# Kernel tuning notes

Hardware: AMD Instinct MI355X
Metric: run time of the kernel (lower is better)

Reference implementation:

```python
import jax, jax.numpy as jnp
import numpy as np

C = 512
NUM_HEADS = 8
RF = 4          # reduction_factor
GROUPS = 8      # min(8, C//8)
EPS = 1e-5


def _pos_enc(h, w, c):
    # matches torch _create_positional_encoding; c must be divisible by 4
    y = jnp.arange(h, dtype=jnp.float32)[:, None] * jnp.ones((1, w), jnp.float32)
    x = jnp.ones((h, 1), jnp.float32) * jnp.arange(w, dtype=jnp.float32)[None, :]
    div = jnp.exp(jnp.arange(0, c // 2, 2, dtype=jnp.float32) * (-np.log(10000.0) / (c // 2)))  # [c//4]
    d = div[:, None, None]
    sy, cy = jnp.sin(y[None] * d), jnp.cos(y[None] * d)   # [c//4,h,w]
    sx, cx = jnp.sin(x[None] * d), jnp.cos(x[None] * d)
    pe = jnp.stack([sy, cy, sx, cx], axis=1).reshape(c, h, w)  # interleaved 0::4..3::4
    return pe[None] * 0.01


def _group_norm(x, w, b):
    B, Cc, H, W = x.shape
    g = x.reshape(B, GROUPS, -1)
    m = g.mean(-1, keepdims=True)
    v = g.var(-1, keepdims=True)
    g = (g - m) / jnp.sqrt(v + EPS)
    return g.reshape(B, Cc, H, W) * w[None, :, None, None] + b[None, :, None, None]


def setup_inputs() -> dict:
    key = jax.random.key(0)
    ks = jax.random.split(key, 4)
    B, H, W = 1, 256, 256
    x = jax.random.normal(ks[0], (B, C, H, W), jnp.float32)
    qkv_w = jax.random.normal(ks[1], (3 * C, C), jnp.float32) * 0.02
    proj_w = jax.random.normal(ks[2], (C, C), jnp.float32) * 0.02
    gamma = jax.random.normal(ks[3], (1,), jnp.float32)
    return {
        "x": x,
        "gn_weight": jnp.ones((C,), jnp.float32),
        "gn_bias": jnp.zeros((C,), jnp.float32),
        "qkv_w": qkv_w,
        "proj_w": proj_w,
        "proj_b": jnp.zeros((C,), jnp.float32),
        "gamma": gamma,
        "temperature": jnp.ones((NUM_HEADS, 1, 1), jnp.float32),
    }


def reference(x, gn_weight, gn_bias, qkv_w, proj_w, proj_b, gamma, temperature):
    B, Cc, H, W = x.shape
    hd = Cc // NUM_HEADS
    identity = x
    xn = _group_norm(x, gn_weight, gn_bias)
    # spatial reduction (AvgPool2d k=4 s=4); H,W > 32 in this config
    Hr, Wr = H // RF, W // RF
    xr = xn.reshape(B, Cc, Hr, RF, Wr, RF).mean(axis=(3, 5))
    xr = xr + _pos_enc(Hr, Wr, Cc)
    qkv = jnp.einsum('oc,bchw->bohw', qkv_w, xr)  # 1x1 conv, no bias
    q, k, v = jnp.split(qkv, 3, axis=1)
    N = Hr * Wr
    q = q.reshape(B, NUM_HEADS, hd, N) * (hd ** -0.5) * temperature[None]
    k = k.reshape(B, NUM_HEADS, hd, N)
    v = v.reshape(B, NUM_HEADS, hd, N)
    # chunked attention in torch == plain softmax attention (chunking over queries)
    attn = jax.nn.softmax(jnp.einsum('bhdn,bhdm->bhnm', q, k), axis=-1)
    out = jnp.einsum('bhnm,bhdm->bhdn', attn, v).reshape(B, Cc, Hr, Wr)
    out = jax.image.resize(out, (B, Cc, H, W), method='bilinear')  # align_corners=False
    out = jnp.einsum('oc,bchw->bohw', proj_w, out) + proj_b[None, :, None, None]
    # dropout in eval mode is identity
    return identity + gamma * out
```

## Files before the change

### kernel.cpp

```cpp
#include <hip/hip_runtime.h>
#include <hip/hip_bf16.h>


typedef __attribute__((ext_vector_type(4))) short short4v;
typedef __attribute__((ext_vector_type(8))) short short8v;
typedef __attribute__((ext_vector_type(4))) float f32x4;
typedef __attribute__((ext_vector_type(4))) unsigned int u32x4;

#define MFMA16(a, b, c) __builtin_amdgcn_mfma_f32_16x16x32_bf16(a, b, c, 0, 0, 0)

__device__ __forceinline__ unsigned short bf16r(float f) {
    unsigned int u = __builtin_bit_cast(unsigned int, f);
    u += 0x7fffu + ((u >> 16) & 1u);
    return (unsigned short)(u >> 16);
}
__device__ __forceinline__ float bff(unsigned short s) {
    unsigned int u = ((unsigned int)s) << 16;
    return __builtin_bit_cast(float, u);
}
__device__ __forceinline__ unsigned int fbits(float f) {
    return __builtin_bit_cast(unsigned int, f);
}

typedef const __attribute__((address_space(1))) unsigned int guint;
typedef __attribute__((address_space(3))) unsigned int luint;
__device__ __forceinline__ void gload16(const void* g, void* l) {
    __builtin_amdgcn_global_load_lds((guint*)g, (luint*)l, 16, 0, 0);
}

__global__ __launch_bounds__(256) void k_wconv(const float* __restrict__ qkv_w,
                                               const float* __restrict__ proj_w,
                                               const float* __restrict__ temp,
                                               unsigned short* __restrict__ wq_b,
                                               unsigned short* __restrict__ wp_b) {
    int idx = blockIdx.x * 256 + threadIdx.x;
    const int NQ = 1536 * 512;
    if (idx < NQ) {
        int o = idx >> 9;
        float sc = (o < 512) ? temp[o >> 6] * 0.125f : 1.0f;
        wq_b[idx] = bf16r(qkv_w[idx] * sc);
    } else {
        int j = idx - NQ;
        wp_b[j] = bf16r(proj_w[j]);
    }
}

__global__ __launch_bounds__(256) void k_pool(const float* __restrict__ x,
                                              float* __restrict__ xp,
                                              float* __restrict__ partials) {
    int hr = blockIdx.x;
    int c  = blockIdx.y;
    int t = threadIdx.x;
    int r = t >> 6, wq = t & 63;
    const float4* src = (const float4*)(x + (size_t)c * 65536 + (size_t)(4 * hr + r) * 256 + 4 * wq);
    float4 v = *src;
    float s4 = v.x + v.y + v.z + v.w;
    float q4 = v.x * v.x + v.y * v.y + v.z * v.z + v.w * v.w;

    __shared__ float sm[256];
    __shared__ float wq4[4];
    sm[t] = s4;
    float qq = q4;
#pragma unroll
    for (int off = 1; off < 64; off <<= 1) qq += __shfl_xor(qq, off, 64);
    if ((t & 63) == 0) wq4[t >> 6] = qq;
    __syncthreads();
    if (t < 64) {
        float cs = sm[t] + sm[64 + t] + sm[128 + t] + sm[192 + t];
        xp[(size_t)c * 4096 + hr * 64 + t] = cs * (1.0f / 16.0f);
        float ts = cs;
#pragma unroll
        for (int off = 1; off < 64; off <<= 1) ts += __shfl_xor(ts, off, 64);
        if (t == 0) {
            int g = c >> 6;
            int slot = (c & 63) * 64 + hr;
            partials[(size_t)(g * 4096 + slot) * 2 + 0] = ts;
            partials[(size_t)(g * 4096 + slot) * 2 + 1] = wq4[0] + wq4[1] + wq4[2] + wq4[3];
        }
    }
}

__global__ __launch_bounds__(256) void k_stats(const float* __restrict__ partials,
                                               float* __restrict__ gstats) {
    int g = blockIdx.x;
    int t = threadIdx.x;
    float s = 0.f, q = 0.f;
    for (int i = t; i < 4096; i += 256) {
        s += partials[(size_t)(g * 4096 + i) * 2 + 0];
        q += partials[(size_t)(g * 4096 + i) * 2 + 1];
    }
#pragma unroll
    for (int off = 1; off < 64; off <<= 1) {
        s += __shfl_xor(s, off, 64);
        q += __shfl_xor(q, off, 64);
    }
    __shared__ float ss[4], qs[4];
    if ((t & 63) == 0) { ss[t >> 6] = s; qs[t >> 6] = q; }
    __syncthreads();
    if (t == 0) {
        float S = ss[0] + ss[1] + ss[2] + ss[3];
        float Q = qs[0] + qs[1] + qs[2] + qs[3];
        const float inv = 1.0f / 4194304.0f;
        float m = S * inv;
        float var = Q * inv - m * m;
        gstats[2 * g] = m;
        gstats[2 * g + 1] = rsqrtf(var + 1e-5f);
    }
}

__global__ __launch_bounds__(256) void k_xr(const float* __restrict__ xp,
                                            const float* __restrict__ gs,
                                            const float* __restrict__ gw,
                                            const float* __restrict__ gb,
                                            unsigned short* __restrict__ xr) {
    int idx = blockIdx.x * 256 + threadIdx.x;
    int c = idx >> 12, n = idx & 4095;
    int hr = n >> 6, wr = n & 63;
    int g = c >> 6;
    float m = gs[2 * g], rs = gs[2 * g + 1];
    float xn = (xp[idx] - m) * rs * gw[c] + gb[c];
    int i = c >> 2, kind = c & 3;
    float di = expf(-(float)i * 0.07195578415606394f);
    float arg = ((kind < 2) ? (float)hr : (float)wr) * di;
    float pe = 0.01f * ((kind & 1) ? cosf(arg) : sinf(arg));
    xr[idx] = bf16r(xn + pe);
}

__global__ __launch_bounds__(256) void k_gemm(const unsigned short* __restrict__ A,
                                              const unsigned short* __restrict__ B,
                                              unsigned short* __restrict__ C) {
    __shared__ unsigned short As[128][36];
    __shared__ unsigned short Bs[128][36];
    int t = threadIdx.x;
    int w = t >> 6, l = t & 63, l15 = l & 15, lg = l >> 4;
    int wrow = w >> 1, wcol = w & 1;
    int m0 = blockIdx.y * 128, n0 = blockIdx.x * 128;
    f32x4 acc[4][4] = {};

    for (int k0 = 0; k0 < 512; k0 += 32) {
#pragma unroll
        for (int i = 0; i < 4; i++) {
            int idx = t + 256 * i;
            int row = idx >> 3, kc = idx & 7;
            short4v av = *(const short4v*)(A + (size_t)(m0 + row) * 512 + k0 + 4 * kc);
            *(short4v*)&As[row][4 * kc] = av;
        }
#pragma unroll
        for (int i = 0; i < 4; i++) {
            int idx = t + 256 * i;
            int kr = idx >> 5, nc = idx & 31;
            short4v bv = *(const short4v*)(B + (size_t)(k0 + kr) * 4096 + n0 + 4 * nc);
#pragma unroll
            for (int j = 0; j < 4; j++) Bs[4 * nc + j][kr] = (unsigned short)bv[j];
        }
        __syncthreads();

        short8v af[4];
#pragma unroll
        for (int mi = 0; mi < 4; mi++) {
            int ar = wrow * 64 + mi * 16 + l15;
            short4v a0 = *(const short4v*)&As[ar][4 * lg];
            short4v a1 = *(const short4v*)&As[ar][16 + 4 * lg];
            af[mi] = __builtin_shufflevector(a0, a1, 0, 1, 2, 3, 4, 5, 6, 7);
        }
#pragma unroll
        for (int ni = 0; ni < 4; ni++) {
            int bc = wcol * 64 + ni * 16 + l15;
            short4v b0 = *(const short4v*)&Bs[bc][4 * lg];
            short4v b1 = *(const short4v*)&Bs[bc][16 + 4 * lg];
            short8v bf = __builtin_shufflevector(b0, b1, 0, 1, 2, 3, 4, 5, 6, 7);
#pragma unroll
            for (int mi = 0; mi < 4; mi++) acc[mi][ni] = MFMA16(af[mi], bf, acc[mi][ni]);
        }
        __syncthreads();
    }
#pragma unroll
    for (int mi = 0; mi < 4; mi++)
#pragma unroll
        for (int ni = 0; ni < 4; ni++) {
            int row = m0 + wrow * 64 + mi * 16 + 4 * lg;
            int col = n0 + wcol * 64 + ni * 16 + l15;
#pragma unroll
            for (int r = 0; r < 4; r++)
                C[(size_t)(row + r) * 4096 + col] = bf16r(acc[mi][ni][r]);
        }
}

__global__ __launch_bounds__(256) void k_perm(const unsigned short* __restrict__ qkv,
                                              unsigned short* __restrict__ qtg,
                                              unsigned short* __restrict__ ktg,
                                              unsigned short* __restrict__ vtg) {
    __shared__ unsigned short lt[64][40];
    int t = threadIdx.x;
    int tile = blockIdx.x, h = blockIdx.y, z = blockIdx.z;
    int base = (z == 0 ? 0 : (z == 1 ? 512 : 1024)) + h * 64;
    int r = t >> 2, c4 = (t & 3) * 8;
    *(short8v*)&lt[r][c4] = *(const short8v*)(qkv + (size_t)(base + r) * 4096 + tile * 32 + c4);
    __syncthreads();
    unsigned short o[8];
    if (z < 2) {
        int col = t & 31, lgc = (t >> 5) & 3, s = t >> 7;
#pragma unroll
        for (int j = 0; j < 4; j++) {
            o[j] = lt[s * 32 + 4 * lgc + j][col];
            o[4 + j] = lt[s * 32 + 16 + 4 * lgc + j][col];
        }
    } else {
        int d = t & 63, lgc = t >> 6;
#pragma unroll
        for (int j = 0; j < 4; j++) {
            o[j] = lt[d][4 * lgc + j];
            o[4 + j] = lt[d][16 + 4 * lgc + j];
        }
    }
    unsigned short* dst = (z == 0 ? qtg : (z == 1 ? ktg : vtg)) + ((size_t)h * 128 + tile) * 2048 + t * 8;
    *(short8v*)dst = *(const short8v*)o;
}

__global__ __launch_bounds__(512) void k_attn(const unsigned short* __restrict__ qtg,
                                              const unsigned short* __restrict__ ktg,
                                              const unsigned short* __restrict__ vtg,
                                              unsigned short* __restrict__ opart,
                                              float* __restrict__ lgl) {
    __shared__ __align__(16) unsigned short kbuf[2][2048];
    __shared__ __align__(16) unsigned short vbuf[2][2048];
    int t = threadIdx.x;
    int l = t & 63, l15 = l & 15, lg = l >> 4, w = t >> 6;
    int qt = blockIdx.x, h = blockIdx.y, seg = blockIdx.z;
    int nu = qt * 8 + w;

    const unsigned short* qb = qtg + ((size_t)h * 128 + nu) * 2048;
    const unsigned short* kb = ktg + ((size_t)h * 128 + seg * 16) * 2048;
    const unsigned short* vb = vtg + ((size_t)h * 128 + seg * 16) * 2048;

    short8v qf[2][2];
#pragma unroll
    for (int ng = 0; ng < 2; ng++)
#pragma unroll
        for (int s = 0; s < 2; s++)
            qf[ng][s] = *(const short8v*)(qb + s * 1024 + lg * 256 + ng * 128 + l15 * 8);

    int st = t & 255;
    const unsigned short* sp = ((t >= 256) ? vb : kb) + st * 8;
    unsigned short* ldst = ((t >= 256) ? &vbuf[0][0] : &kbuf[0][0]) + st * 8;

    f32x4 od[2][4] = {};
    float lsum[2] = {0.f, 0.f};
    const float LOG2E = 1.44269504f;

#define STAGE(kt, u) gload16(sp + (kt) * 2048, ldst + (u) * 2048)

    STAGE(0, 0);

    int u = 0;
#pragma unroll 1
    for (int kt = 0; kt < 16; kt++) {
        if (kt < 15) {
            STAGE(kt + 1, u ^ 1);
            asm volatile("s_waitcnt vmcnt(1)" ::: "memory");
        } else {
            asm volatile("s_waitcnt vmcnt(0)" ::: "memory");
        }
        __builtin_amdgcn_s_barrier();

        const unsigned short* kl = &kbuf[u][0];
        const unsigned short* vl = &vbuf[u][0];

        short8v kf[2][2], vf[4];
#pragma unroll
        for (int mf = 0; mf < 2; mf++)
#pragma unroll
            for (int s = 0; s < 2; s++)
                kf[mf][s] = *(const short8v*)(kl + s * 1024 + lg * 256 + mf * 128 + l15 * 8);
#pragma unroll
        for (int dg = 0; dg < 4; dg++)
            vf[dg] = *(const short8v*)(vl + lg * 512 + dg * 128 + l15 * 8);

#pragma unroll
        for (int ng = 0; ng < 2; ng++) {
            f32x4 s0 = {}, s1 = {};
            __builtin_amdgcn_s_setprio(1);
            s0 = MFMA16(kf[0][0], qf[ng][0], s0);
            s0 = MFMA16(kf[0][1], qf[ng][1], s0);
            s1 = MFMA16(kf[1][0], qf[ng][0], s1);
            s1 = MFMA16(kf[1][1], qf[ng][1], s1);
            __builtin_amdgcn_s_setprio(0);

            float p0[4], p1[4];
#pragma unroll
            for (int r = 0; r < 4; r++) {
                p0[r] = __builtin_amdgcn_exp2f(s0[r] * LOG2E);
                p1[r] = __builtin_amdgcn_exp2f(s1[r] * LOG2E);
            }
            lsum[ng] += ((p0[0] + p0[1]) + (p0[2] + p0[3])) +
                        ((p1[0] + p1[1]) + (p1[2] + p1[3]));

            u32x4 P;
            P[0] = __builtin_amdgcn_perm(fbits(p0[1]), fbits(p0[0]), 0x07060302u);
            P[1] = __builtin_amdgcn_perm(fbits(p0[3]), fbits(p0[2]), 0x07060302u);
            P[2] = __builtin_amdgcn_perm(fbits(p1[1]), fbits(p1[0]), 0x07060302u);
            P[3] = __builtin_amdgcn_perm(fbits(p1[3]), fbits(p1[2]), 0x07060302u);
            short8v pb = __builtin_bit_cast(short8v, P);

            __builtin_amdgcn_s_setprio(1);
#pragma unroll
            for (int dg = 0; dg < 4; dg++) od[ng][dg] = MFMA16(vf[dg], pb, od[ng][dg]);
            __builtin_amdgcn_s_setprio(0);
        }

        __builtin_amdgcn_s_barrier();
        u ^= 1;
    }
#undef STAGE

#pragma unroll
    for (int ng = 0; ng < 2; ng++) {
        lsum[ng] += __shfl_xor(lsum[ng], 16, 64);
        lsum[ng] += __shfl_xor(lsum[ng], 32, 64);
    }

    unsigned short* op = opart + ((size_t)(seg * 512 + h * 64)) * 4096 + nu * 32;
#pragma unroll
    for (int ng = 0; ng < 2; ng++)
#pragma unroll
        for (int dg = 0; dg < 4; dg++)
#pragma unroll
            for (int r = 0; r < 4; r++) {
                int d = dg * 16 + 4 * lg + r;
                op[(size_t)d * 4096 + ng * 16 + l15] = bf16r(od[ng][dg][r]);
            }
    if (lg == 0) {
#pragma unroll
        for (int ng = 0; ng < 2; ng++)
            lgl[(size_t)(seg * 8 + h) * 4096 + nu * 32 + ng * 16 + l15] = lsum[ng];
    }
}

__global__ __launch_bounds__(256) void k_merge(const unsigned short* __restrict__ opart,
                                               const float* __restrict__ lgl,
                                               unsigned short* __restrict__ attn_b) {
    int bid = blockIdx.x, t = threadIdx.x;
    int row = bid >> 2;
    int n0 = (bid & 3) * 1024 + t * 4;
    int h = row >> 6;

    f32x4 den = {};
    float num[4] = {};
#pragma unroll
    for (int s = 0; s < 8; s++) {
        f32x4 lv = *(const f32x4*)(lgl + (size_t)(s * 8 + h) * 4096 + n0);
        den += lv;
        short4v ov = *(const short4v*)(opart + (size_t)s * 2097152 + (size_t)row * 4096 + n0);
#pragma unroll
        for (int j = 0; j < 4; j++) num[j] += bff((unsigned short)ov[j]);
    }
    unsigned short res[4];
#pragma unroll
    for (int j = 0; j < 4; j++) res[j] = bf16r(num[j] / den[j]);
    *(short4v*)(attn_b + (size_t)row * 4096 + n0) = *(const short4v*)res;
}

__global__ __launch_bounds__(256) void k_up(const float* __restrict__ x,
                                            const unsigned short* __restrict__ low,
                                            const float* __restrict__ proj_b,
                                            const float* __restrict__ gamma,
                                            float* __restrict__ out) {
    int t = threadIdx.x;
    int hs = t >> 6;
    int hh = blockIdx.x * 4 + hs;
    int c = blockIdx.y;
    int a = t & 63;

    int ph = hh & 3, Ah = hh >> 2;
    int y0 = Ah + ((ph < 2) ? -1 : 0);
    float fy = (ph < 2) ? (0.625f + 0.25f * ph) : (0.125f + 0.25f * (ph - 2));
    int y1 = min(y0 + 1, 63); y0 = max(y0, 0);

    const unsigned short* L0 = low + (size_t)c * 4096 + y0 * 64;
    const unsigned short* L1 = low + (size_t)c * 4096 + y1 * 64;
    int am = max(a - 1, 0), ap = min(a + 1, 63);
    float gy = 1.f - fy;
    float vm = gy * bff(L0[am]) + fy * bff(L1[am]);
    float v0 = gy * bff(L0[a])  + fy * bff(L1[a]);
    float vp = gy * bff(L0[ap]) + fy * bff(L1[ap]);

    float pb = proj_b[c], g = gamma[0];
    size_t idx = (size_t)c * 65536 + (size_t)hh * 256 + a * 4;
    float4 xi = *(const float4*)(x + idx);
    float4 o;
    o.x = xi.x + g * (0.375f * vm + 0.625f * v0 + pb);
    o.y = xi.y + g * (0.125f * vm + 0.875f * v0 + pb);
    o.z = xi.z + g * (0.875f * v0 + 0.125f * vp + pb);
    o.w = xi.w + g * (0.625f * v0 + 0.375f * vp + pb);
    *(float4*)(out + idx) = o;
}

extern "C" void kernel_launch(void* const* d_in, const int* in_sizes, int n_in,
                              void* d_out, int out_size, void* d_ws, size_t ws_size,
                              hipStream_t stream) {
    const float* x     = (const float*)d_in[0];
    const float* gnw   = (const float*)d_in[1];
    const float* gnb   = (const float*)d_in[2];
    const float* qkvw  = (const float*)d_in[3];
    const float* projw = (const float*)d_in[4];
    const float* projb = (const float*)d_in[5];
    const float* gamma = (const float*)d_in[6];
    const float* temp  = (const float*)d_in[7];

    char* ws = (char*)d_ws;
    const size_t MB = 1u << 20;
    float* gstats          = (float*)(ws + 0);
    float* partials        = (float*)(ws + 1024);
    float* xp              = (float*)(ws + 1 * MB);
    unsigned short* qtg    = (unsigned short*)(ws + 1 * MB);
    unsigned short* ktg    = (unsigned short*)(ws + 5 * MB);
    unsigned short* xr_b   = (unsigned short*)(ws + 9 * MB);
    unsigned short* vtg    = (unsigned short*)(ws + 9 * MB);
    unsigned short* wq_b   = (unsigned short*)(ws + 13 * MB);
    unsigned short* wp_b   = (unsigned short*)(ws + 15 * MB);
    unsigned short* qkv_b  = (unsigned short*)(ws + 16 * MB);
    unsigned short* attn_b = (unsigned short*)(ws + 28 * MB);
    unsigned short* low_b  = (unsigned short*)(ws + 32 * MB);
    float* out = (float*)d_out;
    unsigned short* opart = (unsigned short*)d_out;
    float* lgl = (float*)((char*)d_out + 32 * MB);

    k_wconv<<<4096, 256, 0, stream>>>(qkvw, projw, temp, wq_b, wp_b);
    k_pool<<<dim3(64, 512), 256, 0, stream>>>(x, xp, partials);
    k_stats<<<8, 256, 0, stream>>>(partials, gstats);
    k_xr<<<8192, 256, 0, stream>>>(xp, gstats, gnw, gnb, xr_b);
    k_gemm<<<dim3(32, 12), 256, 0, stream>>>(wq_b, xr_b, qkv_b);
    k_perm<<<dim3(128, 8, 3), 256, 0, stream>>>(qkv_b, qtg, ktg, vtg);
    k_attn<<<dim3(16, 8, 8), 512, 0, stream>>>(qtg, ktg, vtg, opart, lgl);
    k_merge<<<2048, 256, 0, stream>>>(opart, lgl, attn_b);
    k_gemm<<<dim3(32, 4), 256, 0, stream>>>(wp_b, attn_b, low_b);
    k_up<<<dim3(64, 512), 256, 0, stream>>>(x, low_b, projb, gamma, out);
}
```

Measured before the change: 189.4 us.

## Enlarge attention K/V tiles to 64 keys with triple-buffered async loads

```diff
diff --git a/kernel.cpp b/kernel.cpp
--- a/kernel.cpp
+++ b/kernel.cpp
@@ -37,7 +37,7 @@
     const int NQ = 1536 * 512;
     if (idx < NQ) {
         int o = idx >> 9;
-        float sc = (o < 512) ? temp[o >> 6] * 0.125f : 1.0f;
+        float sc = (o < 512) ? temp[o >> 6] * 0.125f * 1.44269504f : 1.0f;
         wq_b[idx] = bf16r(qkv_w[idx] * sc);
     } else {
         int j = idx - NQ;
@@ -190,126 +190,155 @@
                                               unsigned short* __restrict__ qtg,
                                               unsigned short* __restrict__ ktg,
                                               unsigned short* __restrict__ vtg) {
-    __shared__ unsigned short lt[64][40];
+    __shared__ unsigned short lt[64][72];
     int t = threadIdx.x;
     int tile = blockIdx.x, h = blockIdx.y, z = blockIdx.z;
     int base = (z == 0 ? 0 : (z == 1 ? 512 : 1024)) + h * 64;
-    int r = t >> 2, c4 = (t & 3) * 8;
-    *(short8v*)&lt[r][c4] = *(const short8v*)(qkv + (size_t)(base + r) * 4096 + tile * 32 + c4);
+#pragma unroll
+    for (int i = 0; i < 2; i++) {
+        int idx = t + 256 * i;
+        int row = idx >> 3, sg = idx & 7;
+        *(short8v*)&lt[row][sg * 8] =
+            *(const short8v*)(qkv + (size_t)(base + row) * 4096 + tile * 64 + sg * 8);
+    }
     __syncthreads();
-    unsigned short o[8];
-    if (z < 2) {
-        int col = t & 31, lgc = (t >> 5) & 3, s = t >> 7;
-#pragma unroll
-        for (int j = 0; j < 4; j++) {
-            o[j] = lt[s * 32 + 4 * lgc + j][col];
-            o[4 + j] = lt[s * 32 + 16 + 4 * lgc + j][col];
-        }
-    } else {
-        int d = t & 63, lgc = t >> 6;
-#pragma unroll
-        for (int j = 0; j < 4; j++) {
-            o[j] = lt[d][4 * lgc + j];
-            o[4 + j] = lt[d][16 + 4 * lgc + j];
-        }
-    }
-    unsigned short* dst = (z == 0 ? qtg : (z == 1 ? ktg : vtg)) + ((size_t)h * 128 + tile) * 2048 + t * 8;
-    *(short8v*)dst = *(const short8v*)o;
-}
-
-__global__ __launch_bounds__(512) void k_attn(const unsigned short* __restrict__ qtg,
-                                              const unsigned short* __restrict__ ktg,
-                                              const unsigned short* __restrict__ vtg,
-                                              unsigned short* __restrict__ opart,
-                                              float* __restrict__ lgl) {
-    __shared__ __align__(16) unsigned short kbuf[2][2048];
-    __shared__ __align__(16) unsigned short vbuf[2][2048];
+#pragma unroll
+    for (int i = 0; i < 2; i++) {
+        int c = t + 256 * i;
+        unsigned short o[8];
+        unsigned short* dst;
+        if (z == 0) {
+            int nh = c >> 8, cl = c & 255;
+            int s = cl >> 7, lgc = (cl >> 5) & 3, col = cl & 31;
+#pragma unroll
+            for (int j = 0; j < 4; j++) {
+                o[j] = lt[s * 32 + 4 * lgc + j][nh * 32 + col];
+                o[4 + j] = lt[s * 32 + 16 + 4 * lgc + j][nh * 32 + col];
+            }
+            dst = qtg + ((size_t)(h * 128 + tile * 2 + nh)) * 2048 + cl * 8;
+        } else if (z == 1) {
+            int s = c >> 8, lgc = (c >> 6) & 3, m = c & 63;
+#pragma unroll
+            for (int j = 0; j < 4; j++) {
+                o[j] = lt[s * 32 + 4 * lgc + j][m];
+                o[4 + j] = lt[s * 32 + 16 + 4 * lgc + j][m];
+            }
+            dst = ktg + ((size_t)(h * 64 + tile)) * 4096 + c * 8;
+        } else {
+            int mh = c >> 8, lgc = (c >> 6) & 3, d = c & 63;
+#pragma unroll
+            for (int j = 0; j < 4; j++) {
+                o[j] = lt[d][mh * 32 + 4 * lgc + j];
+                o[4 + j] = lt[d][mh * 32 + 16 + 4 * lgc + j];
+            }
+            dst = vtg + ((size_t)(h * 64 + tile)) * 4096 + c * 8;
+        }
+        *(short8v*)dst = *(const short8v*)o;
+    }
+}
+
+__global__ __launch_bounds__(512, 4) void k_attn(const unsigned short* __restrict__ qtg,
+                                                 const unsigned short* __restrict__ ktg,
+                                                 const unsigned short* __restrict__ vtg,
+                                                 unsigned short* __restrict__ opart,
+                                                 float* __restrict__ lgl) {
+    __shared__ __align__(16) unsigned short kbuf[3][4096];
+    __shared__ __align__(16) unsigned short vbuf[3][4096];
     int t = threadIdx.x;
     int l = t & 63, l15 = l & 15, lg = l >> 4, w = t >> 6;
     int qt = blockIdx.x, h = blockIdx.y, seg = blockIdx.z;
     int nu = qt * 8 + w;
 
-    const unsigned short* qb = qtg + ((size_t)h * 128 + nu) * 2048;
-    const unsigned short* kb = ktg + ((size_t)h * 128 + seg * 16) * 2048;
-    const unsigned short* vb = vtg + ((size_t)h * 128 + seg * 16) * 2048;
+    const unsigned short* qb = qtg + ((size_t)(h * 128 + nu)) * 2048;
+    const unsigned short* kb = ktg + ((size_t)(h * 64 + seg * 8)) * 4096;
+    const unsigned short* vb = vtg + ((size_t)(h * 64 + seg * 8)) * 4096;
 
     short8v qf[2][2];
 #pragma unroll
     for (int ng = 0; ng < 2; ng++)
 #pragma unroll
         for (int s = 0; s < 2; s++)
-            qf[ng][s] = *(const short8v*)(qb + s * 1024 + lg * 256 + ng * 128 + l15 * 8);
+            qf[ng][s] = *(const short8v*)(qb + ((s * 4 + lg) * 32 + ng * 16 + l15) * 8);
 
     int st = t & 255;
     const unsigned short* sp = ((t >= 256) ? vb : kb) + st * 8;
-    unsigned short* ldst = ((t >= 256) ? &vbuf[0][0] : &kbuf[0][0]) + st * 8;
+    unsigned short* ld0 = ((t >= 256) ? &vbuf[0][0] : &kbuf[0][0]) + st * 8;
 
     f32x4 od[2][4] = {};
     float lsum[2] = {0.f, 0.f};
-    const float LOG2E = 1.44269504f;
-
-#define STAGE(kt, u) gload16(sp + (kt) * 2048, ldst + (u) * 2048)
+
+#define STAGE(kt, b)                                      \
+    {                                                     \
+        gload16(sp + (kt) * 4096, ld0 + (b) * 4096);      \
+        gload16(sp + (kt) * 4096 + 2048, ld0 + (b) * 4096 + 2048); \
+    }
 
     STAGE(0, 0);
-
-    int u = 0;
+    STAGE(1, 1);
+
+    int cur = 0, nxt = 2;
 #pragma unroll 1
-    for (int kt = 0; kt < 16; kt++) {
-        if (kt < 15) {
-            STAGE(kt + 1, u ^ 1);
-            asm volatile("s_waitcnt vmcnt(1)" ::: "memory");
+    for (int j = 0; j < 8; j++) {
+        if (j < 7) {
+            asm volatile("s_waitcnt vmcnt(2)" ::: "memory");
         } else {
             asm volatile("s_waitcnt vmcnt(0)" ::: "memory");
         }
         __builtin_amdgcn_s_barrier();
-
-        const unsigned short* kl = &kbuf[u][0];
-        const unsigned short* vl = &vbuf[u][0];
-
-        short8v kf[2][2], vf[4];
-#pragma unroll
-        for (int mf = 0; mf < 2; mf++)
-#pragma unroll
-            for (int s = 0; s < 2; s++)
-                kf[mf][s] = *(const short8v*)(kl + s * 1024 + lg * 256 + mf * 128 + l15 * 8);
-#pragma unroll
-        for (int dg = 0; dg < 4; dg++)
-            vf[dg] = *(const short8v*)(vl + lg * 512 + dg * 128 + l15 * 8);
-
-#pragma unroll
-        for (int ng = 0; ng < 2; ng++) {
+        __builtin_amdgcn_sched_barrier(0);
+        if (j < 6) STAGE(j + 2, nxt);
+
+        const unsigned short* kl = &kbuf[0][0] + cur * 4096;
+        const unsigned short* vl = &vbuf[0][0] + cur * 4096;
+
+        short8v pb[2][2];
+        float p[2][2][4];
+#pragma unroll
+        for (int mf = 0; mf < 4; mf++) {
+            short8v k0 = *(const short8v*)(kl + ((0 + lg) * 64 + mf * 16 + l15) * 8);
+            short8v k1 = *(const short8v*)(kl + ((4 + lg) * 64 + mf * 16 + l15) * 8);
             f32x4 s0 = {}, s1 = {};
             __builtin_amdgcn_s_setprio(1);
-            s0 = MFMA16(kf[0][0], qf[ng][0], s0);
-            s0 = MFMA16(kf[0][1], qf[ng][1], s0);
-            s1 = MFMA16(kf[1][0], qf[ng][0], s1);
-            s1 = MFMA16(kf[1][1], qf[ng][1], s1);
+            s0 = MFMA16(k0, qf[0][0], s0);
+            s0 = MFMA16(k1, qf[0][1], s0);
+            s1 = MFMA16(k0, qf[1][0], s1);
+            s1 = MFMA16(k1, qf[1][1], s1);
             __builtin_amdgcn_s_setprio(0);
-
-            float p0[4], p1[4];
+            int half = mf & 1;
 #pragma unroll
             for (int r = 0; r < 4; r++) {
-                p0[r] = __builtin_amdgcn_exp2f(s0[r] * LOG2E);
-                p1[r] = __builtin_amdgcn_exp2f(s1[r] * LOG2E);
-            }
-            lsum[ng] += ((p0[0] + p0[1]) + (p0[2] + p0[3])) +
-                        ((p1[0] + p1[1]) + (p1[2] + p1[3]));
-
-            u32x4 P;
-            P[0] = __builtin_amdgcn_perm(fbits(p0[1]), fbits(p0[0]), 0x07060302u);
-            P[1] = __builtin_amdgcn_perm(fbits(p0[3]), fbits(p0[2]), 0x07060302u);
-            P[2] = __builtin_amdgcn_perm(fbits(p1[1]), fbits(p1[0]), 0x07060302u);
-            P[3] = __builtin_amdgcn_perm(fbits(p1[3]), fbits(p1[2]), 0x07060302u);
-            short8v pb = __builtin_bit_cast(short8v, P);
-
-            __builtin_amdgcn_s_setprio(1);
-#pragma unroll
-            for (int dg = 0; dg < 4; dg++) od[ng][dg] = MFMA16(vf[dg], pb, od[ng][dg]);
-            __builtin_amdgcn_s_setprio(0);
-        }
-
-        __builtin_amdgcn_s_barrier();
-        u ^= 1;
+                p[0][half][r] = __builtin_amdgcn_exp2f(s0[r]);
+                p[1][half][r] = __builtin_amdgcn_exp2f(s1[r]);
+            }
+            lsum[0] += (p[0][half][0] + p[0][half][1]) + (p[0][half][2] + p[0][half][3]);
+            lsum[1] += (p[1][half][0] + p[1][half][1]) + (p[1][half][2] + p[1][half][3]);
+            if (half) {
+                int mh = mf >> 1;
+#pragma unroll
+                for (int ng = 0; ng < 2; ng++) {
+                    u32x4 P;
+                    P[0] = __builtin_amdgcn_perm(fbits(p[ng][0][1]), fbits(p[ng][0][0]), 0x07060302u);
+                    P[1] = __builtin_amdgcn_perm(fbits(p[ng][0][3]), fbits(p[ng][0][2]), 0x07060302u);
+                    P[2] = __builtin_amdgcn_perm(fbits(p[ng][1][1]), fbits(p[ng][1][0]), 0x07060302u);
+                    P[3] = __builtin_amdgcn_perm(fbits(p[ng][1][3]), fbits(p[ng][1][2]), 0x07060302u);
+                    pb[ng][mh] = __builtin_bit_cast(short8v, P);
+                }
+            }
+        }
+
+        __builtin_amdgcn_s_setprio(1);
+#pragma unroll
+        for (int mh = 0; mh < 2; mh++)
+#pragma unroll
+            for (int dg = 0; dg < 4; dg++) {
+                short8v vf = *(const short8v*)(vl + ((mh * 4 + lg) * 64 + dg * 16 + l15) * 8);
+                od[0][dg] = MFMA16(vf, pb[0][mh], od[0][dg]);
+                od[1][dg] = MFMA16(vf, pb[1][mh], od[1][dg]);
+            }
+        __builtin_amdgcn_s_setprio(0);
+
+        cur = (cur == 2) ? 0 : cur + 1;
+        nxt = (nxt == 2) ? 0 : nxt + 1;
     }
 #undef STAGE
 
@@ -430,7 +459,7 @@
     k_stats<<<8, 256, 0, stream>>>(partials, gstats);
     k_xr<<<8192, 256, 0, stream>>>(xp, gstats, gnw, gnb, xr_b);
     k_gemm<<<dim3(32, 12), 256, 0, stream>>>(wq_b, xr_b, qkv_b);
-    k_perm<<<dim3(128, 8, 3), 256, 0, stream>>>(qkv_b, qtg, ktg, vtg);
+    k_perm<<<dim3(64, 8, 3), 256, 0, stream>>>(qkv_b, qtg, ktg, vtg);
     k_attn<<<dim3(16, 8, 8), 512, 0, stream>>>(qtg, ktg, vtg, opart, lgl);
     k_merge<<<2048, 256, 0, stream>>>(opart, lgl, attn_b);
     k_gemm<<<dim3(32, 4), 256, 0, stream>>>(wp_b, attn_b, low_b);
```

Result: no change. 190.0 us (+0.3%).
